# Kernel tuning notes

Hardware: AMD Instinct MI355X
Metric: run time of the kernel (lower is better)

Reference implementation:

```python
import jax, jax.numpy as jnp
import numpy as np

N = 8192; E = 262144
CS = 384; CZ = 128; CH = 16; H = 12; PQK = 4; PV = 8
INF = 1e5; EPS = 1e-8
S_QK = float(1.0 / np.sqrt(3.0 * CH))        # sqrt(1/(3*c_hidden))
S_B = float(1.0 / np.sqrt(3.0))              # sqrt(1/3)
S_PT = float(1.0 / np.sqrt(3.0 * (PQK * 9.0 / 2.0)))


def setup_inputs() -> dict:
    key = jax.random.key(0)
    ks = jax.random.split(key, 16)
    def w(k, shape, fan_in):
        return jax.random.normal(k, shape, jnp.float32) * (1.0 / float(np.sqrt(fan_in)))
    d = {}
    d["s"] = jax.random.normal(ks[0], (N, CS), jnp.float32)
    d["z"] = jax.random.normal(ks[1], (E, CZ), jnp.float32)
    d["edge_index"] = jax.random.randint(ks[2], (2, E), 0, N, jnp.int32)
    d["rot"] = jax.random.normal(ks[3], (N, 3, 3), jnp.float32)
    d["trans"] = jax.random.normal(ks[4], (N, 3), jnp.float32)
    d["mask"] = jnp.ones((N,), jnp.float32)
    d["q_w"] = w(ks[5], (CS, H * CH), CS);              d["q_b"] = jnp.zeros((H * CH,), jnp.float32)
    d["kv_w"] = w(ks[6], (CS, 2 * H * CH), CS);         d["kv_b"] = jnp.zeros((2 * H * CH,), jnp.float32)
    d["qp_w"] = w(ks[7], (CS, H * PQK * 3), CS);        d["qp_b"] = jnp.zeros((H * PQK * 3,), jnp.float32)
    d["kvp_w"] = w(ks[8], (CS, H * (PQK + PV) * 3), CS); d["kvp_b"] = jnp.zeros((H * (PQK + PV) * 3,), jnp.float32)
    d["b_w"] = w(ks[9], (CZ, H), CZ);                   d["b_b"] = jnp.zeros((H,), jnp.float32)
    d["dz_w"] = w(ks[10], (CZ, CZ // 4), CZ);           d["dz_b"] = jnp.zeros((CZ // 4,), jnp.float32)
    d["head_weights"] = jnp.full((H,), float(np.log(np.e - 1.0)), jnp.float32)
    cdim = H * (CZ // 4 + CH + PV * 4)
    d["out_w"] = w(ks[11], (cdim, CS), cdim);           d["out_b"] = jnp.zeros((CS,), jnp.float32)
    return d


def reference(s, z, edge_index, rot, trans, mask,
              q_w, q_b, kv_w, kv_b, qp_w, qp_b, kvp_w, kvp_b,
              b_w, b_b, dz_w, dz_b, head_weights, out_w, out_b):
    src = edge_index[1]
    dst = edge_index[0]

    def to_pts(y, P):
        # y: [N, H*P*3] -> split into (x,y,z) chunks -> [N, H*P, 3], then rigid-apply
        xyz = jnp.stack(jnp.split(y, 3, axis=-1), axis=-1)          # [N, H*P, 3]
        pts = jnp.einsum('nij,npj->npi', rot, xyz) + trans[:, None, :]
        return pts.reshape(N, H, P, 3)

    q = (s @ q_w + q_b).reshape(N, H, CH)
    kv = (s @ kv_w + kv_b).reshape(N, H, 2 * CH)
    k, v = kv[..., :CH], kv[..., CH:]

    q_pts = to_pts(s @ qp_w + qp_b, PQK)                            # [N,H,PQK,3]
    kv_pts = to_pts(s @ kvp_w + kvp_b, PQK + PV)                    # [N,H,PQK+PV,3]
    k_pts, v_pts = kv_pts[..., :PQK, :], kv_pts[..., PQK:, :]

    b = z @ b_w + b_b                                               # [E, H]

    # scalar attention logits
    a = jnp.einsum('ehc,ehc->eh', q[src], k[dst]) * S_QK + S_B * b  # [E, H]

    # point attention logits
    disp = q_pts[src] - k_pts[dst]                                  # [E,H,PQK,3]
    pt_att = jnp.sum(disp * disp, axis=-1)                          # [E,H,PQK]
    hw = jax.nn.softplus(head_weights) * S_PT                       # [H]
    pt_att = -0.5 * jnp.sum(pt_att * hw[None, :, None], axis=-1)    # [E,H]

    edge_mask = INF * (mask[dst] * mask[src] - 1.0)                 # [E]
    a = a + pt_att + edge_mask[:, None]

    # scatter softmax over src segments (pyg-style)
    amax = jax.ops.segment_max(a, src, num_segments=N)
    amax = jnp.where(jnp.isfinite(amax), amax, 0.0)
    ex = jnp.exp(a - amax[src])
    denom = jax.ops.segment_sum(ex, src, num_segments=N)
    a = ex / (denom[src] + 1e-16)                                   # [E,H]

    # weighted scatter-reduce aggregations
    o = jax.ops.segment_sum(a[..., None] * v[dst], src, num_segments=N).reshape(N, H * CH)
    o_pt = jax.ops.segment_sum(a[..., None, None] * v_pts[dst], src, num_segments=N)  # [N,H,PV,3]
    # invert_apply: R^T (p - t)
    o_pt = jnp.einsum('nji,nhpj->nhpi', rot, o_pt - trans[:, None, None, :])
    o_pt_norm = jnp.sqrt(jnp.sum(o_pt * o_pt, axis=-1) + EPS).reshape(N, H * PV)
    o_pt_flat = o_pt.reshape(N, H * PV, 3)

    pair_z = z @ dz_w + dz_b                                        # [E, CZ//4]
    o_pair = jax.ops.segment_sum(a[..., None] * pair_z[:, None, :], src, num_segments=N).reshape(N, H * (CZ // 4))

    feats = jnp.concatenate(
        [o, o_pt_flat[..., 0], o_pt_flat[..., 1], o_pt_flat[..., 2], o_pt_norm, o_pair], axis=-1)
    return feats @ out_w + out_b
```

## Files before the change

### kernel.cpp

```cpp
#include <hip/hip_runtime.h>
#include <math.h>

#define NN 8192
#define EE 262144
#define CSD 384
#define CZD 128
#define HH 12
#define MAXDEG 96
#define ABLD 13

#define S_QK 0.14433756729740643f
#define S_B  0.5773502691896258f
#define S_PT 0.1360827634879543f

typedef __bf16 bf16;
typedef __attribute__((ext_vector_type(8))) __bf16 bf16x8;
typedef __attribute__((ext_vector_type(4))) __bf16 bf16x4;
typedef __attribute__((ext_vector_type(4))) float floatx4;

#define OFF_LIN    0
#define OFF_QPACK  (OFF_LIN + NN*1152)
#define OFF_KPACKH (OFF_QPACK + NN*336)
#define OFF_VPACKH (OFF_KPACKH + NN*192)
#define OFF_BLOG   (OFF_VPACKH + NN*240)
#define OFF_PAIRH  (OFF_BLOG + EE*12)
#define OFF_SBF    (OFF_PAIRH + EE*16)
#define OFF_WCAT   (OFF_SBF + NN*192)
#define OFF_OWT    (OFF_WCAT + 221184)
#define OFF_FEATB  (OFF_OWT + 184320)
#define OFF_BZW    (OFF_FEATB + NN*480)
#define OFF_BZB    (OFF_BZW + 3072)
#define OFF_BIASC  (OFF_BZB + 48)
#define OFF_INTS   (OFF_BIASC + 1152)

__global__ void count_kernel(const int* __restrict__ ei, int* __restrict__ counts) {
    int e = blockIdx.x * 256 + threadIdx.x;
    if (e < EE) atomicAdd(&counts[ei[EE + e]], 1);
}

__global__ __launch_bounds__(1024) void scan_kernel(const int* __restrict__ counts,
                                                    int* __restrict__ offs,
                                                    int* __restrict__ cursor) {
    __shared__ int part[1024];
    int t = threadIdx.x;
    int local[8];
    int s = 0;
    #pragma unroll
    for (int j = 0; j < 8; ++j) { local[j] = counts[t * 8 + j]; s += local[j]; }
    part[t] = s;
    __syncthreads();
    for (int off = 1; off < 1024; off <<= 1) {
        int vv = 0;
        if (t >= off) vv = part[t - off];
        __syncthreads();
        if (t >= off) part[t] += vv;
        __syncthreads();
    }
    int run = (t == 0) ? 0 : part[t - 1];
    #pragma unroll
    for (int j = 0; j < 8; ++j) {
        offs[t * 8 + j] = run;
        cursor[t * 8 + j] = run;
        run += local[j];
    }
    if (t == 1023) offs[NN] = run;
}

__global__ void fill_kernel(const int* __restrict__ ei, int* __restrict__ cursor,
                            int* __restrict__ elist) {
    int e = blockIdx.x * 256 + threadIdx.x;
    if (e < EE) {
        int s = ei[EE + e];
        int pos = atomicAdd(&cursor[s], 1);
        elist[pos] = e;
    }
}

__global__ __launch_bounds__(1024) void sort_kernel(const int* __restrict__ offs,
                                                    int* __restrict__ order) {
    __shared__ int hist[256];
    __shared__ int base[256];
    int t = threadIdx.x;
    if (t < 256) hist[t] = 0;
    __syncthreads();
    for (int n = t; n < NN; n += 1024) {
        int d = offs[n + 1] - offs[n];
        if (d > 255) d = 255;
        atomicAdd(&hist[d], 1);
    }
    __syncthreads();
    if (t == 0) {
        int run = 0;
        for (int d = 255; d >= 0; --d) { base[d] = run; run += hist[d]; }
    }
    __syncthreads();
    for (int n = t; n < NN; n += 1024) {
        int d = offs[n + 1] - offs[n];
        if (d > 255) d = 255;
        int pos = atomicAdd(&base[d], 1);
        order[pos] = n;
    }
}

__global__ void cvt_s_kernel(const float* __restrict__ s, bf16* __restrict__ sbf) {
    int i = blockIdx.x * 256 + threadIdx.x;
    float4 v = *(const float4*)(s + (long)i * 4);
    bf16x4 o = {(__bf16)v.x, (__bf16)v.y, (__bf16)v.z, (__bf16)v.w};
    *(bf16x4*)(sbf + (long)i * 4) = o;
}

__global__ void build_wcat(const float* __restrict__ q_w, const float* __restrict__ kv_w,
                           const float* __restrict__ qp_w, const float* __restrict__ kvp_w,
                           const float* __restrict__ q_b, const float* __restrict__ kv_b,
                           const float* __restrict__ qp_b, const float* __restrict__ kvp_b,
                           bf16* __restrict__ wt, float* __restrict__ bias_cat) {
    int id = blockIdx.x * 256 + threadIdx.x;
    if (id >= 1152 * 384) return;
    int n = id / 384, k = id - n * 384;
    float v;
    if (n < 192)      v = q_w[k * 192 + n];
    else if (n < 576) v = kv_w[k * 384 + (n - 192)];
    else if (n < 720) v = qp_w[k * 144 + (n - 576)];
    else              v = kvp_w[k * 432 + (n - 720)];
    wt[id] = (__bf16)v;
    if (k == 0) {
        float b;
        if (n < 192)      b = q_b[n];
        else if (n < 576) b = kv_b[n - 192];
        else if (n < 720) b = qp_b[n - 576];
        else              b = kvp_b[n - 720];
        bias_cat[n] = b;
    }
}

__global__ void build_owt(const float* __restrict__ out_w, bf16* __restrict__ wt) {
    int id = blockIdx.x * 256 + threadIdx.x;
    if (id >= 384 * 960) return;
    int n = id / 960, k = id - n * 960;
    wt[id] = (__bf16)out_w[k * 384 + n];
}

__global__ void build_bzw(const float* __restrict__ b_w, const float* __restrict__ b_b,
                          const float* __restrict__ dz_w, const float* __restrict__ dz_b,
                          bf16* __restrict__ wt, float* __restrict__ bias) {
    int id = blockIdx.x * 256 + threadIdx.x;
    if (id < 48 * 128) {
        int c = id / 128, k = id - c * 128;
        float v = 0.f;
        if (c < 12)      v = b_w[k * 12 + c];
        else if (c < 44) v = dz_w[k * 32 + (c - 12)];
        wt[id] = (__bf16)v;
    }
    if (id < 44) bias[id] = (id < 12) ? b_b[id] : dz_b[id - 12];
}

#define LDKP 40
__global__ __launch_bounds__(256) void gemm_mfma_bt(const bf16* __restrict__ A,
                                                    const bf16* __restrict__ BT,
                                                    const float* __restrict__ bias,
                                                    float* __restrict__ C,
                                                    int M, int K, int N) {
    __shared__ __align__(16) bf16 As[128][LDKP];
    __shared__ __align__(16) bf16 Bs[128][LDKP];
    const int tid = threadIdx.x;
    const int bm = blockIdx.y * 128;
    const int bn = blockIdx.x * 128;
    const int wave = tid >> 6, lane = tid & 63;
    const int wr = (wave >> 1) * 64;
    const int wc = (wave & 1) * 64;
    const int lm = lane & 15;
    const int kg = lane >> 4;

    floatx4 acc[4][4];
    #pragma unroll
    for (int i = 0; i < 4; ++i)
        #pragma unroll
        for (int j = 0; j < 4; ++j) acc[i][j] = (floatx4){0.f, 0.f, 0.f, 0.f};

    const int srow = tid >> 2;
    const int skoff = (tid & 3) * 8;

    for (int k0 = 0; k0 < K; k0 += 32) {
        __syncthreads();
        *(float4*)(&As[srow][skoff])      = *(const float4*)(A + (long)(bm + srow) * K + k0 + skoff);
        *(float4*)(&As[srow + 64][skoff]) = *(const float4*)(A + (long)(bm + srow + 64) * K + k0 + skoff);
        *(float4*)(&Bs[srow][skoff])      = *(const float4*)(BT + (long)(bn + srow) * K + k0 + skoff);
        *(float4*)(&Bs[srow + 64][skoff]) = *(const float4*)(BT + (long)(bn + srow + 64) * K + k0 + skoff);
        __syncthreads();
        bf16x8 af[4], bfr[4];
        #pragma unroll
        for (int i = 0; i < 4; ++i) af[i] = *(const bf16x8*)(&As[wr + i * 16 + lm][kg * 8]);
        #pragma unroll
        for (int j = 0; j < 4; ++j) bfr[j] = *(const bf16x8*)(&Bs[wc + j * 16 + lm][kg * 8]);
        #pragma unroll
        for (int i = 0; i < 4; ++i)
            #pragma unroll
            for (int j = 0; j < 4; ++j)
                acc[i][j] = __builtin_amdgcn_mfma_f32_16x16x32_bf16(af[i], bfr[j], acc[i][j], 0, 0, 0);
    }

    const int crow0 = bm + wr + kg * 4;
    const int ccol0 = bn + wc + lm;
    #pragma unroll
    for (int i = 0; i < 4; ++i) {
        #pragma unroll
        for (int j = 0; j < 4; ++j) {
            int col = ccol0 + j * 16;
            float b = bias[col];
            #pragma unroll
            for (int r = 0; r < 4; ++r)
                C[(long)(crow0 + i * 16 + r) * N + col] = acc[i][j][r] + b;
        }
    }
}

__global__ __launch_bounds__(256) void gemm_mfma_bt_n64(const bf16* __restrict__ A,
                                                        const bf16* __restrict__ BT,
                                                        const float* __restrict__ bias,
                                                        float* __restrict__ C,
                                                        int M, int K, int N) {
    __shared__ __align__(16) bf16 As[128][LDKP];
    __shared__ __align__(16) bf16 Bs[64][LDKP];
    const int tid = threadIdx.x;
    const int bm = blockIdx.y * 128;
    const int bn = blockIdx.x * 64;
    const int wave = tid >> 6, lane = tid & 63;
    const int wr = (wave >> 1) * 64;
    const int wc = (wave & 1) * 32;
    const int lm = lane & 15;
    const int kg = lane >> 4;

    floatx4 acc[4][2];
    #pragma unroll
    for (int i = 0; i < 4; ++i)
        #pragma unroll
        for (int j = 0; j < 2; ++j) acc[i][j] = (floatx4){0.f, 0.f, 0.f, 0.f};

    const int srow = tid >> 2;
    const int skoff = (tid & 3) * 8;

    for (int k0 = 0; k0 < K; k0 += 32) {
        __syncthreads();
        *(float4*)(&As[srow][skoff])      = *(const float4*)(A + (long)(bm + srow) * K + k0 + skoff);
        *(float4*)(&As[srow + 64][skoff]) = *(const float4*)(A + (long)(bm + srow + 64) * K + k0 + skoff);
        *(float4*)(&Bs[srow][skoff])      = *(const float4*)(BT + (long)(bn + srow) * K + k0 + skoff);
        __syncthreads();
        bf16x8 af[4], bfr[2];
        #pragma unroll
        for (int i = 0; i < 4; ++i) af[i] = *(const bf16x8*)(&As[wr + i * 16 + lm][kg * 8]);
        #pragma unroll
        for (int j = 0; j < 2; ++j) bfr[j] = *(const bf16x8*)(&Bs[wc + j * 16 + lm][kg * 8]);
        #pragma unroll
        for (int i = 0; i < 4; ++i)
            #pragma unroll
            for (int j = 0; j < 2; ++j)
                acc[i][j] = __builtin_amdgcn_mfma_f32_16x16x32_bf16(af[i], bfr[j], acc[i][j], 0, 0, 0);
    }

    const int crow0 = bm + wr + kg * 4;
    const int ccol0 = bn + wc + lm;
    #pragma unroll
    for (int i = 0; i < 4; ++i) {
        #pragma unroll
        for (int j = 0; j < 2; ++j) {
            int col = ccol0 + j * 16;
            float b = bias[col];
            #pragma unroll
            for (int r = 0; r < 4; ++r)
                C[(long)(crow0 + i * 16 + r) * N + col] = acc[i][j][r] + b;
        }
    }
}

#define BZLD 136
__global__ __launch_bounds__(256) void gemm_bz(const float* __restrict__ z,
                                               const bf16* __restrict__ BT,
                                               const float* __restrict__ bias,
                                               float* __restrict__ blog,
                                               bf16* __restrict__ pairh) {
    __shared__ __align__(16) bf16 Bs[48][BZLD];
    const int tid = threadIdx.x;
    const int bm = blockIdx.x * 128;
    for (int idx = tid; idx < 48 * 16; idx += 256) {
        int r = idx >> 4, seg = idx & 15;
        *(bf16x8*)(&Bs[r][seg * 8]) = *(const bf16x8*)(BT + r * 128 + seg * 8);
    }
    __syncthreads();
    const int wave = tid >> 6, lane = tid & 63;
    const int lm = lane & 15, kg = lane >> 4;
    const int rowbase = wave * 32;
    floatx4 acc[2][3];
    #pragma unroll
    for (int i = 0; i < 2; ++i)
        #pragma unroll
        for (int j = 0; j < 3; ++j) acc[i][j] = (floatx4){0.f, 0.f, 0.f, 0.f};
    #pragma unroll
    for (int ks = 0; ks < 4; ++ks) {
        bf16x8 af[2], bfr[3];
        #pragma unroll
        for (int i = 0; i < 2; ++i) {
            const float* zp = z + (long)(bm + rowbase + i * 16 + lm) * 128 + ks * 32 + kg * 8;
            float4 a0 = *(const float4*)zp;
            float4 a1 = *(const float4*)(zp + 4);
            af[i] = (bf16x8){(__bf16)a0.x, (__bf16)a0.y, (__bf16)a0.z, (__bf16)a0.w,
                             (__bf16)a1.x, (__bf16)a1.y, (__bf16)a1.z, (__bf16)a1.w};
        }
        #pragma unroll
        for (int j = 0; j < 3; ++j) bfr[j] = *(const bf16x8*)(&Bs[j * 16 + lm][ks * 32 + kg * 8]);
        #pragma unroll
        for (int i = 0; i < 2; ++i)
            #pragma unroll
            for (int j = 0; j < 3; ++j)
                acc[i][j] = __builtin_amdgcn_mfma_f32_16x16x32_bf16(af[i], bfr[j], acc[i][j], 0, 0, 0);
    }
    #pragma unroll
    for (int i = 0; i < 2; ++i) {
        int r0 = bm + rowbase + i * 16 + kg * 4;
        #pragma unroll
        for (int j = 0; j < 3; ++j) {
            int col = j * 16 + lm;
            if (col < 12) {
                float b = bias[col];
                #pragma unroll
                for (int r = 0; r < 4; ++r)
                    blog[(long)(r0 + r) * 12 + col] = acc[i][j][r] + b;
            } else if (col < 44) {
                float b = bias[col];
                #pragma unroll
                for (int r = 0; r < 4; ++r)
                    pairh[(long)(r0 + r) * 32 + (col - 12)] = (__bf16)(acc[i][j][r] + b);
            }
        }
    }
}

__global__ void pack_kernel(const float* __restrict__ lin,
                            const float* __restrict__ rot, const float* __restrict__ trans,
                            float* __restrict__ qpack, bf16* __restrict__ kpackh,
                            bf16* __restrict__ vpackh) {
    int n = blockIdx.x;
    int t = threadIdx.x;
    const float* row = lin + (long)n * 1152;
    const float* R = rot + n * 9;
    float tx = trans[n * 3 + 0], ty = trans[n * 3 + 1], tz = trans[n * 3 + 2];
    {
        int h = t >> 4, c = t & 15;
        qpack[(long)n * 336 + h * 28 + c] = row[h * 16 + c];
        kpackh[(long)n * 384 + h * 32 + c] = (__bf16)row[192 + h * 32 + c];
        vpackh[(long)n * 480 + h * 40 + c] = (__bf16)row[192 + h * 32 + 16 + c];
    }
    if (t < 48 && (t & 3) == 0) {
        int h = t >> 2;
        #pragma unroll
        for (int j = 0; j < 4; ++j) kpackh[(long)n * 384 + h * 32 + 28 + j] = (__bf16)0.f;
    }
    float x, y, z;
    if (t < 48) {
        x = row[576 + t]; y = row[624 + t]; z = row[672 + t];
    } else {
        int u = t - 48;
        x = row[720 + u]; y = row[864 + u]; z = row[1008 + u];
    }
    float ox = R[0] * x + R[1] * y + R[2] * z + tx;
    float oy = R[3] * x + R[4] * y + R[5] * z + ty;
    float oz = R[6] * x + R[7] * y + R[8] * z + tz;
    if (t < 48) {
        int h = t >> 2, p = t & 3;
        long b = (long)n * 336 + h * 28 + 16 + p * 3;
        qpack[b] = ox; qpack[b + 1] = oy; qpack[b + 2] = oz;
    } else {
        int u = t - 48;
        int h = u / 12, j = u - h * 12;
        if (j < 4) {
            long b = (long)n * 384 + h * 32 + 16 + j * 3;
            kpackh[b] = (__bf16)ox; kpackh[b + 1] = (__bf16)oy; kpackh[b + 2] = (__bf16)oz;
        } else {
            long b = (long)n * 480 + h * 40 + 16 + (j - 4) * 3;
            vpackh[b] = (__bf16)ox; vpackh[b + 1] = (__bf16)oy; vpackh[b + 2] = (__bf16)oz;
        }
    }
}

__global__ __launch_bounds__(128, 6) void agg_fused(const int* __restrict__ offs,
                                                 const int* __restrict__ elist,
                                                 const int* __restrict__ ei,
                                                 const int* __restrict__ order,
                                                 const float* __restrict__ qpack,
                                                 const bf16* __restrict__ kpackh,
                                                 const bf16* __restrict__ vpackh,
                                                 const float* __restrict__ blog,
                                                 const bf16* __restrict__ pairh,
                                                 const float* __restrict__ mask,
                                                 const float* __restrict__ head_w,
                                                 const float* __restrict__ rot,
                                                 const float* __restrict__ trans,
                                                 bf16* __restrict__ feats) {
    const int wave = threadIdx.x >> 6;
    const int lane = threadIdx.x & 63;
    const int n = order[blockIdx.x * 2 + wave];

    __shared__ float abuf_all[2][MAXDEG * ABLD];
    __shared__ __align__(16) float q_all[2][352];
    __shared__ int smeta_all[2][MAXDEG];
    float* abuf  = abuf_all[wave];
    float* q_s   = q_all[wave];
    int*   smeta = smeta_all[wave];

    const int beg = offs[n];
    int deg = offs[n + 1] - beg;
    if (deg > MAXDEG) deg = MAXDEG;

    for (int idx = lane; idx < 84; idx += 64)
        *(float4*)(&q_s[idx * 4]) = *(const float4*)(qpack + (long)n * 336 + idx * 4);
    if (lane < 12) q_s[336 + lane] = log1pf(expf(head_w[lane])) * S_PT;
    const float msrc = mask[n];

    if (lane < deg) {
        int e = elist[beg + lane];
        int d = ei[e];
        unsigned mb = (mask[d] != 0.f) ? 1u : 0u;
        smeta[lane] = (int)(((unsigned)e << 14) | ((unsigned)d << 1) | mb);
    }
    if (64 + lane < deg) {
        int e = elist[beg + 64 + lane];
        int d = ei[e];
        unsigned mb = (mask[d] != 0.f) ? 1u : 0u;
        smeta[64 + lane] = (int)(((unsigned)e << 14) | ((unsigned)d << 1) | mb);
    }
    __syncthreads();

    for (int idx = lane; idx < deg * 12; idx += 64) {
        int c = idx / 12, h = idx - c * 12;
        const unsigned mm = (unsigned)smeta[c];
        const int e = (int)(mm >> 14);
        const int d = (int)((mm >> 1) & 8191u);
        const float md = (float)(mm & 1u);
        const bf16* khp = kpackh + (long)d * 384 + h * 32;
        bf16x8 k0 = *(const bf16x8*)khp;
        bf16x8 k1 = *(const bf16x8*)(khp + 8);
        bf16x8 p0 = *(const bf16x8*)(khp + 16);
        bf16x8 p1 = *(const bf16x8*)(khp + 24);
        const float* qh = &q_s[h * 28];
        float qk = 0.f, pt = 0.f;
        #pragma unroll
        for (int i = 0; i < 8; ++i) qk += qh[i] * (float)k0[i];
        #pragma unroll
        for (int i = 0; i < 8; ++i) qk += qh[8 + i] * (float)k1[i];
        #pragma unroll
        for (int i = 0; i < 8; ++i) { float dd = qh[16 + i] - (float)p0[i]; pt += dd * dd; }
        #pragma unroll
        for (int i = 0; i < 4; ++i) { float dd = qh[24 + i] - (float)p1[i]; pt += dd * dd; }
        float b = blog[(long)e * 12 + h];
        abuf[c * ABLD + h] = qk * S_QK + S_B * b - 0.5f * q_s[336 + h] * pt
                           + 100000.0f * (msrc * md - 1.0f);
    }
    __syncthreads();

    {
        float lg0[12], lg1[12];
        const bool a0 = lane < deg, a1 = 64 + lane < deg;
        #pragma unroll
        for (int h = 0; h < 12; ++h) {
            lg0[h] = a0 ? abuf[lane * ABLD + h] : -1e30f;
            lg1[h] = a1 ? abuf[(64 + lane) * ABLD + h] : -1e30f;
        }
        #pragma unroll
        for (int h = 0; h < 12; ++h) {
            float mx = fmaxf(lg0[h], lg1[h]);
            #pragma unroll
            for (int off = 32; off > 0; off >>= 1) mx = fmaxf(mx, __shfl_xor(mx, off));
            if (!isfinite(mx)) mx = 0.f;
            float w0 = a0 ? __expf(lg0[h] - mx) : 0.f;
            float w1 = a1 ? __expf(lg1[h] - mx) : 0.f;
            float sm = w0 + w1;
            #pragma unroll
            for (int off = 32; off > 0; off >>= 1) sm += __shfl_xor(sm, off);
            float rl = 1.f / (sm + 1e-16f);
            if (a0) abuf[lane * ABLD + h] = w0 * rl;
            if (a1) abuf[(64 + lane) * ABLD + h] = w1 * rl;
        }
    }
    __syncthreads();

    int hh0, off80;
    bool pr0;
    {
        int slot = lane;
        if (slot < 60) { hh0 = slot / 5; off80 = hh0 * 40 + (slot - hh0 * 5) * 8; pr0 = false; }
        else           { hh0 = 0; off80 = (slot - 60) * 8; pr0 = true; }
    }
    const bool a1v = lane < 44;
    const int hh1 = (lane + 4) >> 2;
    const int off81 = (lane & 3) * 8;

    float acc0[8], acc1[8];
    #pragma unroll
    for (int i = 0; i < 8; ++i) { acc0[i] = 0.f; acc1[i] = 0.f; }

    bf16x8 sA0, sA1, sB0, sB1, sC0, sC1;

#define LOADE(cc, s0, s1) do { \
        unsigned mmq = (unsigned)smeta[cc]; \
        const bf16* vpb = vpackh + (long)((mmq >> 1) & 8191u) * 480; \
        const bf16* ppb = pairh + (long)(mmq >> 14) * 32; \
        s0 = *(const bf16x8*)((pr0 ? ppb : vpb) + off80); \
        if (a1v) s1 = *(const bf16x8*)(ppb + off81); \
    } while (0)

#define ACCUME(cc, s0, s1) do { \
        float w0 = abuf[(cc) * ABLD + hh0]; \
        _Pragma("unroll") for (int i = 0; i < 8; ++i) acc0[i] += w0 * (float)s0[i]; \
        if (a1v) { \
            float w1 = abuf[(cc) * ABLD + hh1]; \
            _Pragma("unroll") for (int i = 0; i < 8; ++i) acc1[i] += w1 * (float)s1[i]; \
        } \
    } while (0)

    if (deg > 0) LOADE(0, sA0, sA1);
    if (deg > 1) LOADE(1, sB0, sB1);
    if (deg > 2) LOADE(2, sC0, sC1);
    int c = 0;
    for (; c + 3 <= deg; c += 3) {
        ACCUME(c, sA0, sA1);
        if (c + 3 < deg) LOADE(c + 3, sA0, sA1);
        ACCUME(c + 1, sB0, sB1);
        if (c + 4 < deg) LOADE(c + 4, sB0, sB1);
        ACCUME(c + 2, sC0, sC1);
        if (c + 5 < deg) LOADE(c + 5, sC0, sC1);
    }
    if (c < deg)     ACCUME(c, sA0, sA1);
    if (c + 1 < deg) ACCUME(c + 1, sB0, sB1);
#undef LOADE
#undef ACCUME

    float* opt_s = q_s;
    {
        int slot = lane;
        if (!pr0) {
            int h = hh0, u = slot - h * 5;
            if (u < 2) {
                bf16* fp = feats + (long)n * 960 + h * 16 + u * 8;
                bf16x4 o1 = {(__bf16)acc0[0], (__bf16)acc0[1], (__bf16)acc0[2], (__bf16)acc0[3]};
                bf16x4 o2 = {(__bf16)acc0[4], (__bf16)acc0[5], (__bf16)acc0[6], (__bf16)acc0[7]};
                *(bf16x4*)fp = o1;
                *(bf16x4*)(fp + 4) = o2;
            } else {
                float* op = &opt_s[h * 24 + (u - 2) * 8];
                *(floatx4*)op = (floatx4){acc0[0], acc0[1], acc0[2], acc0[3]};
                *(floatx4*)(op + 4) = (floatx4){acc0[4], acc0[5], acc0[6], acc0[7]};
            }
        } else {
            int seg = slot - 60;
            bf16* fp = feats + (long)n * 960 + 576 + seg * 8;
            bf16x4 o1 = {(__bf16)acc0[0], (__bf16)acc0[1], (__bf16)acc0[2], (__bf16)acc0[3]};
            bf16x4 o2 = {(__bf16)acc0[4], (__bf16)acc0[5], (__bf16)acc0[6], (__bf16)acc0[7]};
            *(bf16x4*)fp = o1;
            *(bf16x4*)(fp + 4) = o2;
        }
    }
    if (a1v) {
        bf16* fp = feats + (long)n * 960 + 576 + hh1 * 32 + (lane & 3) * 8;
        bf16x4 o1 = {(__bf16)acc1[0], (__bf16)acc1[1], (__bf16)acc1[2], (__bf16)acc1[3]};
        bf16x4 o2 = {(__bf16)acc1[4], (__bf16)acc1[5], (__bf16)acc1[6], (__bf16)acc1[7]};
        *(bf16x4*)fp = o1;
        *(bf16x4*)(fp + 4) = o2;
    }
    __syncthreads();

    const float* R = rot + n * 9;
    float tx = trans[n * 3 + 0], ty = trans[n * 3 + 1], tz = trans[n * 3 + 2];
    for (int idx = lane; idx < 96; idx += 64) {
        int h = idx >> 3, p = idx & 7;
        float x = opt_s[h * 24 + p * 3 + 0] - tx;
        float y = opt_s[h * 24 + p * 3 + 1] - ty;
        float zc = opt_s[h * 24 + p * 3 + 2] - tz;
        float ox = R[0] * x + R[3] * y + R[6] * zc;
        float oy = R[1] * x + R[4] * y + R[7] * zc;
        float oz = R[2] * x + R[5] * y + R[8] * zc;
        float nrm = sqrtf(ox * ox + oy * oy + oz * oz + 1e-8f);
        feats[(long)n * 960 + 192 + idx] = (__bf16)ox;
        feats[(long)n * 960 + 288 + idx] = (__bf16)oy;
        feats[(long)n * 960 + 384 + idx] = (__bf16)oz;
        feats[(long)n * 960 + 480 + idx] = (__bf16)nrm;
    }
}

extern "C" void kernel_launch(void* const* d_in, const int* in_sizes, int n_in,
                              void* d_out, int out_size, void* d_ws, size_t ws_size,
                              hipStream_t stream) {
    const float* s      = (const float*)d_in[0];
    const float* z      = (const float*)d_in[1];
    const int*   ei     = (const int*)d_in[2];
    const float* rot    = (const float*)d_in[3];
    const float* trans  = (const float*)d_in[4];
    const float* mask   = (const float*)d_in[5];
    const float* q_w    = (const float*)d_in[6];
    const float* q_b    = (const float*)d_in[7];
    const float* kv_w   = (const float*)d_in[8];
    const float* kv_b   = (const float*)d_in[9];
    const float* qp_w   = (const float*)d_in[10];
    const float* qp_b   = (const float*)d_in[11];
    const float* kvp_w  = (const float*)d_in[12];
    const float* kvp_b  = (const float*)d_in[13];
    const float* b_w    = (const float*)d_in[14];
    const float* b_b    = (const float*)d_in[15];
    const float* dz_w   = (const float*)d_in[16];
    const float* dz_b   = (const float*)d_in[17];
    const float* head_w = (const float*)d_in[18];
    const float* out_w  = (const float*)d_in[19];
    const float* out_b  = (const float*)d_in[20];

    float* ws      = (float*)d_ws;
    float* lin     = ws + OFF_LIN;
    float* qpack   = ws + OFF_QPACK;
    bf16*  kpackh  = (bf16*)(ws + OFF_KPACKH);
    bf16*  vpackh  = (bf16*)(ws + OFF_VPACKH);
    float* blog    = ws + OFF_BLOG;
    bf16*  pairh   = (bf16*)(ws + OFF_PAIRH);
    bf16*  sbf     = (bf16*)(ws + OFF_SBF);
    bf16*  wcat    = (bf16*)(ws + OFF_WCAT);
    bf16*  owt     = (bf16*)(ws + OFF_OWT);
    bf16*  featb   = (bf16*)(ws + OFF_FEATB);
    bf16*  bzwbf   = (bf16*)(ws + OFF_BZW);
    float* bzb     = ws + OFF_BZB;
    float* biasc   = ws + OFF_BIASC;
    int* ints   = (int*)(ws + OFF_INTS);
    int* offs   = ints;
    int* cursor = ints + NN + 1;
    int* counts = ints + 2 * NN + 1;
    int* elist  = ints + 3 * NN + 1;
    int* order  = ints + 3 * NN + 1 + EE;

    hipMemsetAsync(counts, 0, NN * sizeof(int), stream);
    count_kernel<<<EE / 256, 256, 0, stream>>>(ei, counts);
    scan_kernel<<<1, 1024, 0, stream>>>(counts, offs, cursor);
    fill_kernel<<<EE / 256, 256, 0, stream>>>(ei, cursor, elist);
    sort_kernel<<<1, 1024, 0, stream>>>(offs, order);

    cvt_s_kernel<<<NN * CSD / 4 / 256, 256, 0, stream>>>(s, sbf);
    build_wcat<<<(1152 * 384 + 255) / 256, 256, 0, stream>>>(q_w, kv_w, qp_w, kvp_w,
                                                             q_b, kv_b, qp_b, kvp_b, wcat, biasc);
    build_owt<<<(384 * 960 + 255) / 256, 256, 0, stream>>>(out_w, owt);
    build_bzw<<<(48 * 128 + 255) / 256, 256, 0, stream>>>(b_w, b_b, dz_w, dz_b, bzwbf, bzb);

    gemm_mfma_bt<<<dim3(1152 / 128, NN / 128), 256, 0, stream>>>(sbf, wcat, biasc, lin, NN, CSD, 1152);

    pack_kernel<<<NN, 192, 0, stream>>>(lin, rot, trans, qpack, kpackh, vpackh);

    gemm_bz<<<EE / 128, 256, 0, stream>>>(z, bzwbf, bzb, blog, pairh);

    agg_fused<<<NN / 2, 128, 0, stream>>>(offs, elist, ei, order, qpack, kpackh, vpackh,
                                          blog, pairh, mask, head_w, rot, trans, featb);

    gemm_mfma_bt_n64<<<dim3(384 / 64, NN / 128), 256, 0, stream>>>(featb, owt, out_b, (float*)d_out, NN, 960, 384);
}
```

Measured before the change: 482.9 us.

## Merge prep kernels, fuse fill with sort, use readlane for edge metadata

Merges the input conversion and three weight-repack kernels into a single block-dispatched launch, and merges the edge-list fill with the degree sort into one launch, with the last block doing the sort. This cuts kernel launch and tail overheads in the preprocessing stage. In the aggregation kernel, per-edge metadata is kept in registers and broadcast with readlane instead of being re-read from shared memory. The occupancy hint drops from 6 to 4 waves, which gives the compiler more registers but may reduce latency hiding.

```diff
diff --git a/kernel.cpp b/kernel.cpp
--- a/kernel.cpp
+++ b/kernel.cpp
@@ -66,21 +66,21 @@
     if (t == 1023) offs[NN] = run;
 }
 
-__global__ void fill_kernel(const int* __restrict__ ei, int* __restrict__ cursor,
-                            int* __restrict__ elist) {
-    int e = blockIdx.x * 256 + threadIdx.x;
-    if (e < EE) {
+__global__ __launch_bounds__(1024) void fill_sort(const int* __restrict__ ei,
+                                                  int* __restrict__ cursor,
+                                                  int* __restrict__ elist,
+                                                  const int* __restrict__ offs,
+                                                  int* __restrict__ order) {
+    int t = threadIdx.x;
+    if (blockIdx.x < 256) {
+        int e = blockIdx.x * 1024 + t;
         int s = ei[EE + e];
         int pos = atomicAdd(&cursor[s], 1);
         elist[pos] = e;
-    }
-}
-
-__global__ __launch_bounds__(1024) void sort_kernel(const int* __restrict__ offs,
-                                                    int* __restrict__ order) {
+        return;
+    }
     __shared__ int hist[256];
     __shared__ int base[256];
-    int t = threadIdx.x;
     if (t < 256) hist[t] = 0;
     __syncthreads();
     for (int n = t; n < NN; n += 1024) {
@@ -102,56 +102,54 @@
     }
 }
 
-__global__ void cvt_s_kernel(const float* __restrict__ s, bf16* __restrict__ sbf) {
-    int i = blockIdx.x * 256 + threadIdx.x;
-    float4 v = *(const float4*)(s + (long)i * 4);
-    bf16x4 o = {(__bf16)v.x, (__bf16)v.y, (__bf16)v.z, (__bf16)v.w};
-    *(bf16x4*)(sbf + (long)i * 4) = o;
-}
-
-__global__ void build_wcat(const float* __restrict__ q_w, const float* __restrict__ kv_w,
+__global__ void prep_fused(const float* __restrict__ s, bf16* __restrict__ sbf,
+                           const float* __restrict__ q_w, const float* __restrict__ kv_w,
                            const float* __restrict__ qp_w, const float* __restrict__ kvp_w,
                            const float* __restrict__ q_b, const float* __restrict__ kv_b,
                            const float* __restrict__ qp_b, const float* __restrict__ kvp_b,
-                           bf16* __restrict__ wt, float* __restrict__ bias_cat) {
-    int id = blockIdx.x * 256 + threadIdx.x;
-    if (id >= 1152 * 384) return;
-    int n = id / 384, k = id - n * 384;
-    float v;
-    if (n < 192)      v = q_w[k * 192 + n];
-    else if (n < 576) v = kv_w[k * 384 + (n - 192)];
-    else if (n < 720) v = qp_w[k * 144 + (n - 576)];
-    else              v = kvp_w[k * 432 + (n - 720)];
-    wt[id] = (__bf16)v;
-    if (k == 0) {
-        float b;
-        if (n < 192)      b = q_b[n];
-        else if (n < 576) b = kv_b[n - 192];
-        else if (n < 720) b = qp_b[n - 576];
-        else              b = kvp_b[n - 720];
-        bias_cat[n] = b;
-    }
-}
-
-__global__ void build_owt(const float* __restrict__ out_w, bf16* __restrict__ wt) {
-    int id = blockIdx.x * 256 + threadIdx.x;
-    if (id >= 384 * 960) return;
-    int n = id / 960, k = id - n * 960;
-    wt[id] = (__bf16)out_w[k * 384 + n];
-}
-
-__global__ void build_bzw(const float* __restrict__ b_w, const float* __restrict__ b_b,
-                          const float* __restrict__ dz_w, const float* __restrict__ dz_b,
-                          bf16* __restrict__ wt, float* __restrict__ bias) {
-    int id = blockIdx.x * 256 + threadIdx.x;
-    if (id < 48 * 128) {
-        int c = id / 128, k = id - c * 128;
-        float v = 0.f;
-        if (c < 12)      v = b_w[k * 12 + c];
-        else if (c < 44) v = dz_w[k * 32 + (c - 12)];
-        wt[id] = (__bf16)v;
-    }
-    if (id < 44) bias[id] = (id < 12) ? b_b[id] : dz_b[id - 12];
+                           bf16* __restrict__ wcat, float* __restrict__ bias_cat,
+                           const float* __restrict__ out_w, bf16* __restrict__ owt,
+                           const float* __restrict__ b_w, const float* __restrict__ b_b,
+                           const float* __restrict__ dz_w, const float* __restrict__ dz_b,
+                           bf16* __restrict__ bzw, float* __restrict__ bzb) {
+    int b = blockIdx.x, tid = threadIdx.x;
+    if (b < 3072) {
+        int i = b * 256 + tid;
+        float4 v = *(const float4*)(s + (long)i * 4);
+        bf16x4 o = {(__bf16)v.x, (__bf16)v.y, (__bf16)v.z, (__bf16)v.w};
+        *(bf16x4*)(sbf + (long)i * 4) = o;
+    } else if (b < 4800) {
+        int id = (b - 3072) * 256 + tid;
+        int n = id / 384, k = id - n * 384;
+        float v;
+        if (n < 192)      v = q_w[k * 192 + n];
+        else if (n < 576) v = kv_w[k * 384 + (n - 192)];
+        else if (n < 720) v = qp_w[k * 144 + (n - 576)];
+        else              v = kvp_w[k * 432 + (n - 720)];
+        wcat[id] = (__bf16)v;
+        if (k == 0) {
+            float bb;
+            if (n < 192)      bb = q_b[n];
+            else if (n < 576) bb = kv_b[n - 192];
+            else if (n < 720) bb = qp_b[n - 576];
+            else              bb = kvp_b[n - 720];
+            bias_cat[n] = bb;
+        }
+    } else if (b < 6240) {
+        int id = (b - 4800) * 256 + tid;
+        int n = id / 960, k = id - n * 960;
+        owt[id] = (__bf16)out_w[k * 384 + n];
+    } else {
+        int id = (b - 6240) * 256 + tid;
+        if (id < 48 * 128) {
+            int c = id / 128, k = id - c * 128;
+            float v = 0.f;
+            if (c < 12)      v = b_w[k * 12 + c];
+            else if (c < 44) v = dz_w[k * 32 + (c - 12)];
+            bzw[id] = (__bf16)v;
+        }
+        if (id < 44) bzb[id] = (id < 12) ? b_b[id] : dz_b[id - 12];
+    }
 }
 
 #define LDKP 40
@@ -381,7 +379,7 @@
     }
 }
 
-__global__ __launch_bounds__(128, 6) void agg_fused(const int* __restrict__ offs,
+__global__ __launch_bounds__(128, 4) void agg_fused(const int* __restrict__ offs,
                                                  const int* __restrict__ elist,
                                                  const int* __restrict__ ei,
                                                  const int* __restrict__ order,
@@ -415,17 +413,20 @@
     if (lane < 12) q_s[336 + lane] = log1pf(expf(head_w[lane])) * S_PT;
     const float msrc = mask[n];
 
+    unsigned meta0 = 0u, meta1 = 0u;
     if (lane < deg) {
         int e = elist[beg + lane];
         int d = ei[e];
         unsigned mb = (mask[d] != 0.f) ? 1u : 0u;
-        smeta[lane] = (int)(((unsigned)e << 14) | ((unsigned)d << 1) | mb);
+        meta0 = ((unsigned)e << 14) | ((unsigned)d << 1) | mb;
+        smeta[lane] = (int)meta0;
     }
     if (64 + lane < deg) {
         int e = elist[beg + 64 + lane];
         int d = ei[e];
         unsigned mb = (mask[d] != 0.f) ? 1u : 0u;
-        smeta[64 + lane] = (int)(((unsigned)e << 14) | ((unsigned)d << 1) | mb);
+        meta1 = ((unsigned)e << 14) | ((unsigned)d << 1) | mb;
+        smeta[64 + lane] = (int)meta1;
     }
     __syncthreads();
 
@@ -500,9 +501,10 @@
     bf16x8 sA0, sA1, sB0, sB1, sC0, sC1;
 
 #define LOADE(cc, s0, s1) do { \
-        unsigned mmq = (unsigned)smeta[cc]; \
-        const bf16* vpb = vpackh + (long)((mmq >> 1) & 8191u) * 480; \
-        const bf16* ppb = pairh + (long)(mmq >> 14) * 32; \
+        int mraw = __builtin_amdgcn_readlane((int)(((cc) < 64) ? meta0 : meta1), (cc) & 63); \
+        unsigned um = (unsigned)mraw; \
+        const bf16* vpb = vpackh + (long)((um >> 1) & 8191u) * 480; \
+        const bf16* ppb = pairh + (long)(um >> 14) * 32; \
         s0 = *(const bf16x8*)((pr0 ? ppb : vpb) + off80); \
         if (a1v) s1 = *(const bf16x8*)(ppb + off81); \
     } while (0)
@@ -631,17 +633,14 @@
     int* elist  = ints + 3 * NN + 1;
     int* order  = ints + 3 * NN + 1 + EE;
 
+    prep_fused<<<6264, 256, 0, stream>>>(s, sbf, q_w, kv_w, qp_w, kvp_w,
+                                         q_b, kv_b, qp_b, kvp_b, wcat, biasc,
+                                         out_w, owt, b_w, b_b, dz_w, dz_b, bzwbf, bzb);
+
     hipMemsetAsync(counts, 0, NN * sizeof(int), stream);
     count_kernel<<<EE / 256, 256, 0, stream>>>(ei, counts);
     scan_kernel<<<1, 1024, 0, stream>>>(counts, offs, cursor);
-    fill_kernel<<<EE / 256, 256, 0, stream>>>(ei, cursor, elist);
-    sort_kernel<<<1, 1024, 0, stream>>>(offs, order);
-
-    cvt_s_kernel<<<NN * CSD / 4 / 256, 256, 0, stream>>>(s, sbf);
-    build_wcat<<<(1152 * 384 + 255) / 256, 256, 0, stream>>>(q_w, kv_w, qp_w, kvp_w,
-                                                             q_b, kv_b, qp_b, kvp_b, wcat, biasc);
-    build_owt<<<(384 * 960 + 255) / 256, 256, 0, stream>>>(out_w, owt);
-    build_bzw<<<(48 * 128 + 255) / 256, 256, 0, stream>>>(b_w, b_b, dz_w, dz_b, bzwbf, bzb);
+    fill_sort<<<257, 1024, 0, stream>>>(ei, cursor, elist, offs, order);
 
     gemm_mfma_bt<<<dim3(1152 / 128, NN / 128), 256, 0, stream>>>(sbf, wcat, biasc, lin, NN, CSD, 1152);
 
```

New measurement: 442.6 us. -8.3%, faster.
